# Kernel tuning notes

Measured on AMD Instinct MI355X. Metric: run time of the kernel, lower is better.

Reference implementation:

```python
import jax, jax.numpy as jnp
import numpy as np

B, L_TEXT, N_TOKEN = 8, 2048, 2048
C_TEXT, C_OUT = 3584, 384
C_HID = C_OUT * 2
CHAIN_TYPES = (1, 2)   # heavy, light
CDR_TYPES = (2, 4, 6)  # CDR1/2/3


def setup_inputs() -> dict:
    key = jax.random.key(0)
    ks = jax.random.split(key, 10)
    text_conditioning = jax.random.normal(ks[0], (B, L_TEXT, C_TEXT), jnp.float32)
    text_mask = jnp.ones((B, L_TEXT), jnp.int32)
    chain_type_ids = jax.random.randint(ks[1], (B, L_TEXT), 0, 3).astype(jnp.int32)
    cdr_region_type_ids = jax.random.randint(ks[2], (B, L_TEXT), 0, 10).astype(jnp.int32)
    boltz_chain_type = jax.random.randint(ks[3], (B, N_TOKEN), 0, 4).astype(jnp.int32)
    boltz_region_type = jax.random.randint(ks[4], (B, N_TOKEN), 0, 10).astype(jnp.int32)
    W1 = jax.random.normal(ks[5], (C_HID, C_TEXT), jnp.float32) * 0.02
    b1 = jnp.zeros((C_HID,), jnp.float32)
    W2 = jax.random.normal(ks[6], (C_OUT, C_HID), jnp.float32) * 0.02
    b2 = jnp.zeros((C_OUT,), jnp.float32)
    scale = jnp.ones((1,), jnp.float32)
    return {
        "text_conditioning": text_conditioning, "text_mask": text_mask,
        "chain_type_ids": chain_type_ids, "cdr_region_type_ids": cdr_region_type_ids,
        "boltz_chain_type": boltz_chain_type, "boltz_region_type": boltz_region_type,
        "W1": W1, "b1": b1, "W2": W2, "b2": b2, "scale": scale,
    }


def _align_one(text_proj, tmask, pmask):
    # text_proj: [L, C]; tmask: [L] bool (text CDR positions); pmask: [N] bool (protein CDR positions)
    # The k-th masked text token (in sequence order) maps to the k-th masked protein token,
    # for k < min(n_text, n_protein). Other protein positions get zeros.
    L = tmask.shape[0]
    trank = jnp.cumsum(tmask) - 1          # rank among text CDR tokens
    n_text = jnp.sum(tmask)
    prank = jnp.cumsum(pmask) - 1          # rank among protein CDR tokens
    # idx_by_rank[r] = text index whose rank is r; out-of-range scatter indices dropped
    idx_by_rank = jnp.zeros((L,), jnp.int32).at[jnp.where(tmask, trank, L)].set(
        jnp.arange(L, dtype=jnp.int32), mode="drop")
    valid = pmask & (prank < n_text)       # prank < n_protein holds by construction under pmask
    src = idx_by_rank[jnp.clip(prank, 0, L - 1)]
    emb = text_proj[src]                   # [N, C]
    return jnp.where(valid[:, None], emb, jnp.zeros((), text_proj.dtype))


def reference(text_conditioning, text_mask, chain_type_ids, cdr_region_type_ids,
              boltz_chain_type, boltz_region_type, W1, b1, W2, b2, scale):
    # 2-layer MLP projection: c_text -> 2*c_out -> c_out with SiLU
    h = jax.nn.silu(jnp.einsum("blt,ht->blh", text_conditioning, W1) + b1)
    text_proj = jnp.einsum("blh,ch->blc", h, W2) + b2    # [B, L, C_OUT]

    tm = text_mask.astype(bool)
    result = jnp.zeros((text_conditioning.shape[0], boltz_chain_type.shape[1], W2.shape[0]),
                       text_proj.dtype)
    align = jax.vmap(_align_one)
    for ct in CHAIN_TYPES:
        for rt in CDR_TYPES:
            tmask = (chain_type_ids == ct) & (cdr_region_type_ids == rt) & tm
            pmask = (boltz_chain_type == ct) & (boltz_region_type == rt)
            # (chain, cdr) pairs write to disjoint protein positions, so add is exact
            result = result + align(text_proj, tmask, pmask)
    return scale * result
```

## Files before the change

kernel.cpp:

```cpp
#include <hip/hip_runtime.h>
#include <hip/hip_bf16.h>
#include <math.h>

typedef __bf16 bf16_t;
typedef bf16_t bf16x8 __attribute__((ext_vector_type(8)));
typedef bf16_t bf16x4 __attribute__((ext_vector_type(4)));
typedef float f32x4 __attribute__((ext_vector_type(4)));

#define L_TEXT 2048
#define N_TOKEN 2048
#define C_TEXT 3584
#define C_OUT 384
#define C_HID 768
#define BATCH 8
#define MAXROWS (BATCH * N_TOKEN)
#define PM 3072
#define KSPLIT 4
#define KCHUNK (C_TEXT / KSPLIT)
#define KSPLIT2 2
#define KCHUNK2 (C_HID / KSPLIT2)

#define NW1 (C_HID * C_TEXT / 8)
#define NW2 (C_OUT * C_HID / 8)
#define NINV (MAXROWS / 4)
#define NINIT (NW1 + NW2 + NINV + 1)

__global__ __launch_bounds__(256) void init_cvt_kernel(
    const float* __restrict__ W1, const float* __restrict__ W2,
    bf16_t* __restrict__ W1b, bf16_t* __restrict__ W2b,
    int* __restrict__ inv, int* __restrict__ count) {
    int idx = blockIdx.x * 256 + threadIdx.x;
    if (idx < NW1) {
        int i = idx * 8;
        float4 v0 = *(const float4*)(W1 + i);
        float4 v1 = *(const float4*)(W1 + i + 4);
        bf16x8 o;
        o[0] = (bf16_t)v0.x; o[1] = (bf16_t)v0.y; o[2] = (bf16_t)v0.z; o[3] = (bf16_t)v0.w;
        o[4] = (bf16_t)v1.x; o[5] = (bf16_t)v1.y; o[6] = (bf16_t)v1.z; o[7] = (bf16_t)v1.w;
        *(bf16x8*)(W1b + i) = o;
    } else if (idx < NW1 + NW2) {
        int i = (idx - NW1) * 8;
        float4 v0 = *(const float4*)(W2 + i);
        float4 v1 = *(const float4*)(W2 + i + 4);
        bf16x8 o;
        o[0] = (bf16_t)v0.x; o[1] = (bf16_t)v0.y; o[2] = (bf16_t)v0.z; o[3] = (bf16_t)v0.w;
        o[4] = (bf16_t)v1.x; o[5] = (bf16_t)v1.y; o[6] = (bf16_t)v1.z; o[7] = (bf16_t)v1.w;
        *(bf16x8*)(W2b + i) = o;
    } else if (idx < NW1 + NW2 + NINV) {
        int i = idx - NW1 - NW2;
        int4 m1 = {-1, -1, -1, -1};
        ((int4*)inv)[i] = m1;
    } else if (idx == NW1 + NW2 + NINV) {
        *count = 0;
    }
}

__global__ __launch_bounds__(64) void map_kernel(
    const int* __restrict__ tm, const int* __restrict__ ctid,
    const int* __restrict__ cdrid, const int* __restrict__ bct,
    const int* __restrict__ brt,
    int* __restrict__ rows_src, int* __restrict__ inv,
    int* __restrict__ count) {
    __shared__ int trow[L_TEXT];
    const int bp = blockIdx.x;
    const int b = bp / 6, p = bp % 6;
    const int ct = (p < 3) ? 1 : 2;
    const int rt = 2 + 2 * (p % 3);
    const int lane = threadIdx.x;
    const unsigned long long ltm = (1ull << lane) - 1ull;

    unsigned int tbits = 0, pbits = 0;
#pragma unroll
    for (int i = 0; i < 32; i++) {
        int l = i * 64 + lane;
        unsigned int m = (ctid[b * L_TEXT + l] == ct) &&
                         (cdrid[b * L_TEXT + l] == rt) &&
                         (tm[b * L_TEXT + l] != 0);
        tbits |= m << i;
    }
#pragma unroll
    for (int i = 0; i < 32; i++) {
        int n = i * 64 + lane;
        unsigned int m = (bct[b * N_TOKEN + n] == ct) &&
                         (brt[b * N_TOKEN + n] == rt);
        pbits |= m << i;
    }

    int base = 0;
#pragma unroll
    for (int i = 0; i < 32; i++) {
        bool m = (tbits >> i) & 1;
        unsigned long long bal = __ballot(m);
        if (m) trow[base + __popcll(bal & ltm)] = i * 64 + lane;
        base += __popcll(bal);
    }
    const int n_text = base;
    __syncthreads();

    base = 0;
#pragma unroll
    for (int i = 0; i < 32; i++) {
        bool m = (pbits >> i) & 1;
        unsigned long long bal = __ballot(m);
        if (m) {
            int pr = base + __popcll(bal & ltm);
            if (pr < n_text) {
                int idx = atomicAdd(count, 1);
                if (idx < PM) {
                    rows_src[idx] = b * L_TEXT + trow[pr];
                    inv[b * N_TOKEN + i * 64 + lane] = idx;
                }
            }
        }
        base += __popcll(bal);
    }
}

__global__ __launch_bounds__(256) void gemm1_kernel(
    const float* __restrict__ X, const bf16_t* __restrict__ W1b,
    const int* __restrict__ rows_src, const int* __restrict__ countp,
    float* __restrict__ P) {
    const int count = *countp;
    const int m0 = blockIdx.x * 64;
    if (m0 >= count) return;
    const int n0 = blockIdx.y * 128;
    const int kbeg = blockIdx.z * KCHUNK;

    __shared__ __align__(16) bf16_t As[2][64][40];
    __shared__ __align__(16) bf16_t Bs[2][128][40];

    const int t = threadIdx.x;
    const int lane = t & 63;
    const int w = t >> 6;
    const int wr = w >> 1, wc = w & 1;
    const int fr = lane & 15;
    const int kq = (lane >> 4) * 8;

    f32x4 acc[2][4];
#pragma unroll
    for (int i = 0; i < 2; i++)
#pragma unroll
        for (int j = 0; j < 4; j++) acc[i][j] = (f32x4){0.f, 0.f, 0.f, 0.f};

    const int arow = t >> 2, ac8 = (t & 3) * 8;
    const bool av = (m0 + arow < count);
    const float* ap = X + (size_t)(av ? rows_src[m0 + arow] : 0) * C_TEXT + kbeg + ac8;
    const int aofs = arow * 40 + ac8;
    const bf16_t* bp[2];
    int bofs[2];
#pragma unroll
    for (int j = 0; j < 2; j++) {
        int c = t + 256 * j;
        int row = c >> 2, c8 = (c & 3) * 8;
        bp[j] = W1b + (size_t)(n0 + row) * C_TEXT + kbeg + c8;
        bofs[j] = row * 40 + c8;
    }

    bf16_t* AsF = &As[0][0][0];
    bf16_t* BsF = &Bs[0][0][0];
    const int ABUF = 64 * 40, BBUF = 128 * 40;

    bf16x8 ra, rb0, rb1;
    {
        float4 v0 = *(const float4*)(ap);
        float4 v1 = *(const float4*)(ap + 4);
        ra[0] = (bf16_t)v0.x; ra[1] = (bf16_t)v0.y; ra[2] = (bf16_t)v0.z; ra[3] = (bf16_t)v0.w;
        ra[4] = (bf16_t)v1.x; ra[5] = (bf16_t)v1.y; ra[6] = (bf16_t)v1.z; ra[7] = (bf16_t)v1.w;
        if (!av) { for (int e = 0; e < 8; e++) ra[e] = (bf16_t)0.0f; }
        rb0 = *(const bf16x8*)(bp[0]);
        rb1 = *(const bf16x8*)(bp[1]);
    }

    const int T = KCHUNK / 32;
    for (int tile = 0; tile < T; ++tile) {
        const int cur = tile & 1;
        *(bf16x8*)(AsF + cur * ABUF + aofs) = ra;
        *(bf16x8*)(BsF + cur * BBUF + bofs[0]) = rb0;
        *(bf16x8*)(BsF + cur * BBUF + bofs[1]) = rb1;
        if (tile + 1 < T) {
            int k = (tile + 1) * 32;
            float4 v0 = *(const float4*)(ap + k);
            float4 v1 = *(const float4*)(ap + k + 4);
            bf16x8 na;
            na[0] = (bf16_t)v0.x; na[1] = (bf16_t)v0.y; na[2] = (bf16_t)v0.z; na[3] = (bf16_t)v0.w;
            na[4] = (bf16_t)v1.x; na[5] = (bf16_t)v1.y; na[6] = (bf16_t)v1.z; na[7] = (bf16_t)v1.w;
            if (!av) { for (int e = 0; e < 8; e++) na[e] = (bf16_t)0.0f; }
            bf16x8 nb0 = *(const bf16x8*)(bp[0] + k);
            bf16x8 nb1 = *(const bf16x8*)(bp[1] + k);
            __syncthreads();
            bf16x8 af[2], bfr[4];
#pragma unroll
            for (int mi = 0; mi < 2; mi++)
                af[mi] = *(const bf16x8*)(AsF + cur * ABUF + (wr * 32 + mi * 16 + fr) * 40 + kq);
#pragma unroll
            for (int ni = 0; ni < 4; ni++)
                bfr[ni] = *(const bf16x8*)(BsF + cur * BBUF + (wc * 64 + ni * 16 + fr) * 40 + kq);
#pragma unroll
            for (int mi = 0; mi < 2; mi++)
#pragma unroll
                for (int ni = 0; ni < 4; ni++)
                    acc[mi][ni] = __builtin_amdgcn_mfma_f32_16x16x32_bf16(
                        af[mi], bfr[ni], acc[mi][ni], 0, 0, 0);
            ra = na; rb0 = nb0; rb1 = nb1;
        } else {
            __syncthreads();
            bf16x8 af[2], bfr[4];
#pragma unroll
            for (int mi = 0; mi < 2; mi++)
                af[mi] = *(const bf16x8*)(AsF + cur * ABUF + (wr * 32 + mi * 16 + fr) * 40 + kq);
#pragma unroll
            for (int ni = 0; ni < 4; ni++)
                bfr[ni] = *(const bf16x8*)(BsF + cur * BBUF + (wc * 64 + ni * 16 + fr) * 40 + kq);
#pragma unroll
            for (int mi = 0; mi < 2; mi++)
#pragma unroll
                for (int ni = 0; ni < 4; ni++)
                    acc[mi][ni] = __builtin_amdgcn_mfma_f32_16x16x32_bf16(
                        af[mi], bfr[ni], acc[mi][ni], 0, 0, 0);
        }
    }

    float* Pk = P + (size_t)blockIdx.z * PM * C_HID;
    const int rj = (lane >> 4) * 4;
#pragma unroll
    for (int mi = 0; mi < 2; mi++) {
#pragma unroll
        for (int ni = 0; ni < 4; ni++) {
            int gn = n0 + wc * 64 + ni * 16 + fr;
#pragma unroll
            for (int j = 0; j < 4; j++) {
                int gm = m0 + wr * 32 + mi * 16 + rj + j;
                if (gm < count) Pk[(size_t)gm * C_HID + gn] = acc[mi][ni][j];
            }
        }
    }
}

__global__ __launch_bounds__(256) void reduce1_kernel(
    const float* __restrict__ P, const float* __restrict__ b1,
    const int* __restrict__ countp, bf16_t* __restrict__ H) {
    const int count = *countp;
    int idx = blockIdx.x * 256 + threadIdx.x;
    int m = idx / (C_HID / 4);
    int c = (idx % (C_HID / 4)) * 4;
    if (m >= count) return;
    f32x4 s = *(const f32x4*)(P + (size_t)m * C_HID + c);
#pragma unroll
    for (int ks = 1; ks < KSPLIT; ks++)
        s += *(const f32x4*)(P + ((size_t)ks * PM + m) * C_HID + c);
    f32x4 bb = *(const f32x4*)(b1 + c);
    bf16x4 o;
#pragma unroll
    for (int j = 0; j < 4; j++) {
        float v = s[j] + bb[j];
        o[j] = (bf16_t)(v / (1.0f + __expf(-v)));
    }
    *(bf16x4*)(H + (size_t)m * C_HID + c) = o;
}

__global__ __launch_bounds__(256) void gemm2_kernel(
    const bf16_t* __restrict__ Hm, const bf16_t* __restrict__ W2b,
    const int* __restrict__ countp, float* __restrict__ P2) {
    const int count = *countp;
    const int m0 = blockIdx.x * 64;
    if (m0 >= count) return;
    const int n0 = blockIdx.y * 128;
    const int kbeg = blockIdx.z * KCHUNK2;

    __shared__ __align__(16) bf16_t As[2][64][40];
    __shared__ __align__(16) bf16_t Bs[2][128][40];

    const int t = threadIdx.x;
    const int lane = t & 63;
    const int w = t >> 6;
    const int wr = w >> 1, wc = w & 1;
    const int fr = lane & 15;
    const int kq = (lane >> 4) * 8;

    f32x4 acc[2][4];
#pragma unroll
    for (int i = 0; i < 2; i++)
#pragma unroll
        for (int j = 0; j < 4; j++) acc[i][j] = (f32x4){0.f, 0.f, 0.f, 0.f};

    const int arow = t >> 2, ac8 = (t & 3) * 8;
    const bf16_t* ap = Hm + (size_t)(m0 + arow) * C_HID + kbeg + ac8;
    const int aofs = arow * 40 + ac8;
    const bf16_t* bp[2];
    int bofs[2];
#pragma unroll
    for (int j = 0; j < 2; j++) {
        int c = t + 256 * j;
        int row = c >> 2, c8 = (c & 3) * 8;
        bp[j] = W2b + (size_t)(n0 + row) * C_HID + kbeg + c8;
        bofs[j] = row * 40 + c8;
    }

    bf16_t* AsF = &As[0][0][0];
    bf16_t* BsF = &Bs[0][0][0];
    const int ABUF = 64 * 40, BBUF = 128 * 40;

    bf16x8 ra = *(const bf16x8*)(ap);
    bf16x8 rb0 = *(const bf16x8*)(bp[0]);
    bf16x8 rb1 = *(const bf16x8*)(bp[1]);

    const int T = KCHUNK2 / 32;
    for (int tile = 0; tile < T; ++tile) {
        const int cur = tile & 1;
        *(bf16x8*)(AsF + cur * ABUF + aofs) = ra;
        *(bf16x8*)(BsF + cur * BBUF + bofs[0]) = rb0;
        *(bf16x8*)(BsF + cur * BBUF + bofs[1]) = rb1;
        bf16x8 na, nb0, nb1;
        bool more = (tile + 1 < T);
        if (more) {
            int k = (tile + 1) * 32;
            na = *(const bf16x8*)(ap + k);
            nb0 = *(const bf16x8*)(bp[0] + k);
            nb1 = *(const bf16x8*)(bp[1] + k);
        }
        __syncthreads();
        bf16x8 af[2], bfr[4];
#pragma unroll
        for (int mi = 0; mi < 2; mi++)
            af[mi] = *(const bf16x8*)(AsF + cur * ABUF + (wr * 32 + mi * 16 + fr) * 40 + kq);
#pragma unroll
        for (int ni = 0; ni < 4; ni++)
            bfr[ni] = *(const bf16x8*)(BsF + cur * BBUF + (wc * 64 + ni * 16 + fr) * 40 + kq);
#pragma unroll
        for (int mi = 0; mi < 2; mi++)
#pragma unroll
            for (int ni = 0; ni < 4; ni++)
                acc[mi][ni] = __builtin_amdgcn_mfma_f32_16x16x32_bf16(
                    af[mi], bfr[ni], acc[mi][ni], 0, 0, 0);
        if (more) { ra = na; rb0 = nb0; rb1 = nb1; }
    }

    float* Pk = P2 + (size_t)blockIdx.z * PM * C_OUT;
    const int rj = (lane >> 4) * 4;
#pragma unroll
    for (int mi = 0; mi < 2; mi++) {
#pragma unroll
        for (int ni = 0; ni < 4; ni++) {
            int gn = n0 + wc * 64 + ni * 16 + fr;
#pragma unroll
            for (int j = 0; j < 4; j++) {
                int gm = m0 + wr * 32 + mi * 16 + rj + j;
                if (gm < count) Pk[(size_t)gm * C_OUT + gn] = acc[mi][ni][j];
            }
        }
    }
}

__global__ __launch_bounds__(256) void out_kernel(
    const float* __restrict__ P2, const float* __restrict__ b2,
    const int* __restrict__ inv, const float* __restrict__ scale,
    float* __restrict__ out) {
    int idx = blockIdx.x * 256 + threadIdx.x;
    int token = idx / (C_OUT / 4);
    int c = (idx % (C_OUT / 4)) * 4;
    int m = inv[token];
    f32x4 o = (f32x4){0.f, 0.f, 0.f, 0.f};
    if (m >= 0) {
        f32x4 s = *(const f32x4*)(P2 + (size_t)m * C_OUT + c);
#pragma unroll
        for (int ks = 1; ks < KSPLIT2; ks++)
            s += *(const f32x4*)(P2 + ((size_t)ks * PM + m) * C_OUT + c);
        f32x4 bb = *(const f32x4*)(b2 + c);
        const float sc = scale[0];
#pragma unroll
        for (int j = 0; j < 4; j++) o[j] = sc * (s[j] + bb[j]);
    }
    *(f32x4*)(out + (size_t)token * C_OUT + c) = o;
}

extern "C" void kernel_launch(void* const* d_in, const int* in_sizes, int n_in,
                              void* d_out, int out_size, void* d_ws, size_t ws_size,
                              hipStream_t stream) {
    const float* X     = (const float*)d_in[0];
    const int*   tm    = (const int*)d_in[1];
    const int*   ctid  = (const int*)d_in[2];
    const int*   cdrid = (const int*)d_in[3];
    const int*   bct   = (const int*)d_in[4];
    const int*   brt   = (const int*)d_in[5];
    const float* W1    = (const float*)d_in[6];
    const float* b1    = (const float*)d_in[7];
    const float* W2    = (const float*)d_in[8];
    const float* b2    = (const float*)d_in[9];
    const float* scale = (const float*)d_in[10];

    char* ws = (char*)d_ws;
    size_t off = 0;
    int* count = (int*)(ws + off);        off += 1024;
    int* rows_src = (int*)(ws + off);     off += (size_t)PM * 4;
    int* inv = (int*)(ws + off);          off += (size_t)MAXROWS * 4;
    bf16_t* W1b = (bf16_t*)(ws + off);    off += (size_t)C_HID * C_TEXT * 2;
    bf16_t* W2b = (bf16_t*)(ws + off);    off += (size_t)C_OUT * C_HID * 2;
    bf16_t* H = (bf16_t*)(ws + off);      off += (size_t)PM * C_HID * 2;
    float* P = (float*)(ws + off);        off += (size_t)KSPLIT * PM * C_HID * 4;
    float* P2 = P;

    init_cvt_kernel<<<(NINIT + 255) / 256, 256, 0, stream>>>(W1, W2, W1b, W2b,
                                                             inv, count);

    map_kernel<<<BATCH * 6, 64, 0, stream>>>(tm, ctid, cdrid, bct, brt,
                                             rows_src, inv, count);

    dim3 g1(PM / 64, C_HID / 128, KSPLIT);
    gemm1_kernel<<<g1, 256, 0, stream>>>(X, W1b, rows_src, count, P);

    reduce1_kernel<<<(PM * C_HID / 4) / 256, 256, 0, stream>>>(P, b1, count, H);

    dim3 g2(PM / 64, C_OUT / 128, KSPLIT2);
    gemm2_kernel<<<g2, 256, 0, stream>>>(H, W2b, count, P2);

    out_kernel<<<(MAXROWS * C_OUT / 4) / 256, 256, 0, stream>>>(
        P2, b2, inv, scale, (float*)d_out);
}
```

Baseline: 132.2 us.

## Pre-gather selected text rows to bf16 and enlarge gemm1 M tile to 128

Adds a gather kernel that copies the selected text rows into a compact bf16 buffer once. Before this, every N-tile block of gemm1 re-read and re-converted the fp32 rows. gemm1 then reads bf16 rows directly and uses a 128x128 tile with 4x4 MFMA fragments per wave, which raises arithmetic intensity and halves the number of M blocks. The cost is an extra kernel launch, a bf16 write-then-read round trip for the gathered rows, and more accumulator registers, which may lower occupancy. Count is also clamped to PM across kernels.

```diff
diff --git a/kernel.cpp b/kernel.cpp
--- a/kernel.cpp
+++ b/kernel.cpp
@@ -24,6 +24,7 @@
 #define NW2 (C_OUT * C_HID / 8)
 #define NINV (MAXROWS / 4)
 #define NINIT (NW1 + NW2 + NINV + 1)
+#define GCH (C_TEXT / 8)
 
 __global__ __launch_bounds__(256) void init_cvt_kernel(
     const float* __restrict__ W1, const float* __restrict__ W2,
@@ -116,17 +117,33 @@
     }
 }
 
+__global__ __launch_bounds__(256) void gather_kernel(
+    const float* __restrict__ X, const int* __restrict__ rows_src,
+    const int* __restrict__ countp, bf16_t* __restrict__ Xg) {
+    int count = *countp; if (count > PM) count = PM;
+    int idx = blockIdx.x * 256 + threadIdx.x;
+    int m = idx / GCH;
+    if (m >= count) return;
+    int c = (idx % GCH) * 8;
+    const float* src = X + (size_t)rows_src[m] * C_TEXT + c;
+    float4 v0 = *(const float4*)(src);
+    float4 v1 = *(const float4*)(src + 4);
+    bf16x8 o;
+    o[0] = (bf16_t)v0.x; o[1] = (bf16_t)v0.y; o[2] = (bf16_t)v0.z; o[3] = (bf16_t)v0.w;
+    o[4] = (bf16_t)v1.x; o[5] = (bf16_t)v1.y; o[6] = (bf16_t)v1.z; o[7] = (bf16_t)v1.w;
+    *(bf16x8*)(Xg + (size_t)m * C_TEXT + c) = o;
+}
+
 __global__ __launch_bounds__(256) void gemm1_kernel(
-    const float* __restrict__ X, const bf16_t* __restrict__ W1b,
-    const int* __restrict__ rows_src, const int* __restrict__ countp,
-    float* __restrict__ P) {
-    const int count = *countp;
-    const int m0 = blockIdx.x * 64;
+    const bf16_t* __restrict__ Xg, const bf16_t* __restrict__ W1b,
+    const int* __restrict__ countp, float* __restrict__ P) {
+    int count = *countp; if (count > PM) count = PM;
+    const int m0 = blockIdx.x * 128;
     if (m0 >= count) return;
     const int n0 = blockIdx.y * 128;
     const int kbeg = blockIdx.z * KCHUNK;
 
-    __shared__ __align__(16) bf16_t As[2][64][40];
+    __shared__ __align__(16) bf16_t As[2][128][40];
     __shared__ __align__(16) bf16_t Bs[2][128][40];
 
     const int t = threadIdx.x;
@@ -136,100 +153,80 @@
     const int fr = lane & 15;
     const int kq = (lane >> 4) * 8;
 
-    f32x4 acc[2][4];
-#pragma unroll
-    for (int i = 0; i < 2; i++)
+    f32x4 acc[4][4];
+#pragma unroll
+    for (int i = 0; i < 4; i++)
 #pragma unroll
         for (int j = 0; j < 4; j++) acc[i][j] = (f32x4){0.f, 0.f, 0.f, 0.f};
 
-    const int arow = t >> 2, ac8 = (t & 3) * 8;
-    const bool av = (m0 + arow < count);
-    const float* ap = X + (size_t)(av ? rows_src[m0 + arow] : 0) * C_TEXT + kbeg + ac8;
-    const int aofs = arow * 40 + ac8;
+    const bf16_t* ap[2];
     const bf16_t* bp[2];
-    int bofs[2];
+    int ofs[2];
 #pragma unroll
     for (int j = 0; j < 2; j++) {
         int c = t + 256 * j;
         int row = c >> 2, c8 = (c & 3) * 8;
+        ap[j] = Xg + (size_t)(m0 + row) * C_TEXT + kbeg + c8;
         bp[j] = W1b + (size_t)(n0 + row) * C_TEXT + kbeg + c8;
-        bofs[j] = row * 40 + c8;
+        ofs[j] = row * 40 + c8;
     }
 
     bf16_t* AsF = &As[0][0][0];
     bf16_t* BsF = &Bs[0][0][0];
-    const int ABUF = 64 * 40, BBUF = 128 * 40;
-
-    bf16x8 ra, rb0, rb1;
-    {
-        float4 v0 = *(const float4*)(ap);
-        float4 v1 = *(const float4*)(ap + 4);
-        ra[0] = (bf16_t)v0.x; ra[1] = (bf16_t)v0.y; ra[2] = (bf16_t)v0.z; ra[3] = (bf16_t)v0.w;
-        ra[4] = (bf16_t)v1.x; ra[5] = (bf16_t)v1.y; ra[6] = (bf16_t)v1.z; ra[7] = (bf16_t)v1.w;
-        if (!av) { for (int e = 0; e < 8; e++) ra[e] = (bf16_t)0.0f; }
-        rb0 = *(const bf16x8*)(bp[0]);
-        rb1 = *(const bf16x8*)(bp[1]);
-    }
+    const int BUF = 128 * 40;
+
+    bf16x8 ra[2], rb[2];
+#pragma unroll
+    for (int j = 0; j < 2; j++) { ra[j] = *(const bf16x8*)(ap[j]); rb[j] = *(const bf16x8*)(bp[j]); }
 
     const int T = KCHUNK / 32;
     for (int tile = 0; tile < T; ++tile) {
         const int cur = tile & 1;
-        *(bf16x8*)(AsF + cur * ABUF + aofs) = ra;
-        *(bf16x8*)(BsF + cur * BBUF + bofs[0]) = rb0;
-        *(bf16x8*)(BsF + cur * BBUF + bofs[1]) = rb1;
-        if (tile + 1 < T) {
+#pragma unroll
+        for (int j = 0; j < 2; j++) {
+            *(bf16x8*)(AsF + cur * BUF + ofs[j]) = ra[j];
+            *(bf16x8*)(BsF + cur * BUF + ofs[j]) = rb[j];
+        }
+        bf16x8 na[2], nb[2];
+        bool more = (tile + 1 < T);
+        if (more) {
             int k = (tile + 1) * 32;
-            float4 v0 = *(const float4*)(ap + k);
-            float4 v1 = *(const float4*)(ap + k + 4);
-            bf16x8 na;
-            na[0] = (bf16_t)v0.x; na[1] = (bf16_t)v0.y; na[2] = (bf16_t)v0.z; na[3] = (bf16_t)v0.w;
-            na[4] = (bf16_t)v1.x; na[5] = (bf16_t)v1.y; na[6] = (bf16_t)v1.z; na[7] = (bf16_t)v1.w;
-            if (!av) { for (int e = 0; e < 8; e++) na[e] = (bf16_t)0.0f; }
-            bf16x8 nb0 = *(const bf16x8*)(bp[0] + k);
-            bf16x8 nb1 = *(const bf16x8*)(bp[1] + k);
-            __syncthreads();
-            bf16x8 af[2], bfr[4];
-#pragma unroll
-            for (int mi = 0; mi < 2; mi++)
-                af[mi] = *(const bf16x8*)(AsF + cur * ABUF + (wr * 32 + mi * 16 + fr) * 40 + kq);
+#pragma unroll
+            for (int j = 0; j < 2; j++) {
+                na[j] = *(const bf16x8*)(ap[j] + k);
+                nb[j] = *(const bf16x8*)(bp[j] + k);
+            }
+        }
+        __syncthreads();
+        bf16x8 af[4], bfr[4];
+#pragma unroll
+        for (int mi = 0; mi < 4; mi++)
+            af[mi] = *(const bf16x8*)(AsF + cur * BUF + (wr * 64 + mi * 16 + fr) * 40 + kq);
+#pragma unroll
+        for (int ni = 0; ni < 4; ni++)
+            bfr[ni] = *(const bf16x8*)(BsF + cur * BUF + (wc * 64 + ni * 16 + fr) * 40 + kq);
+#pragma unroll
+        for (int mi = 0; mi < 4; mi++)
 #pragma unroll
             for (int ni = 0; ni < 4; ni++)
-                bfr[ni] = *(const bf16x8*)(BsF + cur * BBUF + (wc * 64 + ni * 16 + fr) * 40 + kq);
-#pragma unroll
-            for (int mi = 0; mi < 2; mi++)
-#pragma unroll
-                for (int ni = 0; ni < 4; ni++)
-                    acc[mi][ni] = __builtin_amdgcn_mfma_f32_16x16x32_bf16(
-                        af[mi], bfr[ni], acc[mi][ni], 0, 0, 0);
-            ra = na; rb0 = nb0; rb1 = nb1;
-        } else {
-            __syncthreads();
-            bf16x8 af[2], bfr[4];
-#pragma unroll
-            for (int mi = 0; mi < 2; mi++)
-                af[mi] = *(const bf16x8*)(AsF + cur * ABUF + (wr * 32 + mi * 16 + fr) * 40 + kq);
-#pragma unroll
-            for (int ni = 0; ni < 4; ni++)
-                bfr[ni] = *(const bf16x8*)(BsF + cur * BBUF + (wc * 64 + ni * 16 + fr) * 40 + kq);
-#pragma unroll
-            for (int mi = 0; mi < 2; mi++)
-#pragma unroll
-                for (int ni = 0; ni < 4; ni++)
-                    acc[mi][ni] = __builtin_amdgcn_mfma_f32_16x16x32_bf16(
-                        af[mi], bfr[ni], acc[mi][ni], 0, 0, 0);
+                acc[mi][ni] = __builtin_amdgcn_mfma_f32_16x16x32_bf16(
+                    af[mi], bfr[ni], acc[mi][ni], 0, 0, 0);
+        if (more) {
+#pragma unroll
+            for (int j = 0; j < 2; j++) { ra[j] = na[j]; rb[j] = nb[j]; }
         }
     }
 
     float* Pk = P + (size_t)blockIdx.z * PM * C_HID;
     const int rj = (lane >> 4) * 4;
 #pragma unroll
-    for (int mi = 0; mi < 2; mi++) {
+    for (int mi = 0; mi < 4; mi++) {
 #pragma unroll
         for (int ni = 0; ni < 4; ni++) {
             int gn = n0 + wc * 64 + ni * 16 + fr;
 #pragma unroll
             for (int j = 0; j < 4; j++) {
-                int gm = m0 + wr * 32 + mi * 16 + rj + j;
+                int gm = m0 + wr * 64 + mi * 16 + rj + j;
                 if (gm < count) Pk[(size_t)gm * C_HID + gn] = acc[mi][ni][j];
             }
         }
@@ -239,7 +236,7 @@
 __global__ __launch_bounds__(256) void reduce1_kernel(
     const float* __restrict__ P, const float* __restrict__ b1,
     const int* __restrict__ countp, bf16_t* __restrict__ H) {
-    const int count = *countp;
+    int count = *countp; if (count > PM) count = PM;
     int idx = blockIdx.x * 256 + threadIdx.x;
     int m = idx / (C_HID / 4);
     int c = (idx % (C_HID / 4)) * 4;
@@ -261,7 +258,7 @@
 __global__ __launch_bounds__(256) void gemm2_kernel(
     const bf16_t* __restrict__ Hm, const bf16_t* __restrict__ W2b,
     const int* __restrict__ countp, float* __restrict__ P2) {
-    const int count = *countp;
+    int count = *countp; if (count > PM) count = PM;
     const int m0 = blockIdx.x * 64;
     if (m0 >= count) return;
     const int n0 = blockIdx.y * 128;
@@ -395,6 +392,7 @@
     int* inv = (int*)(ws + off);          off += (size_t)MAXROWS * 4;
     bf16_t* W1b = (bf16_t*)(ws + off);    off += (size_t)C_HID * C_TEXT * 2;
     bf16_t* W2b = (bf16_t*)(ws + off);    off += (size_t)C_OUT * C_HID * 2;
+    bf16_t* Xg = (bf16_t*)(ws + off);     off += (size_t)PM * C_TEXT * 2;
     bf16_t* H = (bf16_t*)(ws + off);      off += (size_t)PM * C_HID * 2;
     float* P = (float*)(ws + off);        off += (size_t)KSPLIT * PM * C_HID * 4;
     float* P2 = P;
@@ -405,8 +403,10 @@
     map_kernel<<<BATCH * 6, 64, 0, stream>>>(tm, ctid, cdrid, bct, brt,
                                              rows_src, inv, count);
 
-    dim3 g1(PM / 64, C_HID / 128, KSPLIT);
-    gemm1_kernel<<<g1, 256, 0, stream>>>(X, W1b, rows_src, count, P);
+    gather_kernel<<<(PM * GCH) / 256, 256, 0, stream>>>(X, rows_src, count, Xg);
+
+    dim3 g1(PM / 128, C_HID / 128, KSPLIT);
+    gemm1_kernel<<<g1, 256, 0, stream>>>(Xg, W1b, count, P);
 
     reduce1_kernel<<<(PM * C_HID / 4) / 256, 256, 0, stream>>>(P, b1, count, H);
 
```

Measured after the change: 136.1 us. 3.0% more time.
